# Performance work log

Measured on AMD Instinct MI355X. Metric: run time of the kernel, lower is better.

The kernel has to match this reference:

```python
import jax, jax.numpy as jnp
import numpy as np

NB = 50  # nb_steps
IN_D = 64
HID = 128
B = 256


def _cc_weights(nb):
    # Faithful port of UMNN compute_cc_weights (Clenshaw-Curtis quadrature)
    lam = np.arange(0, nb + 1).reshape(-1, 1).astype(np.float64)
    lam = np.cos((lam @ lam.T) * np.pi / nb)
    lam[:, 0] = 0.5
    lam[:, -1] = 0.5 * lam[:, -1]
    lam = lam * 2.0 / nb
    W = np.arange(0, nb + 1).reshape(-1, 1).astype(np.float64)
    W[np.arange(1, nb + 1, 2)] = 0
    W = 2.0 / (1.0 - W ** 2)
    W[0] = 1
    W[np.arange(1, nb + 1, 2)] = 0
    cc = (lam.T @ W)[:, 0].astype(np.float32)              # [nb+1]
    steps = np.cos(np.arange(0, nb + 1) * np.pi / nb).astype(np.float32)  # [nb+1]
    return jnp.asarray(cc), jnp.asarray(steps)


def setup_inputs() -> dict:
    key = jax.random.key(0)
    ks = jax.random.split(key, 16)
    d = {}
    d["x"] = jax.random.normal(ks[0], (B, 1), dtype=jnp.float32)
    d["h"] = jax.random.normal(ks[1], (B, IN_D - 1), dtype=jnp.float32)

    def lin(kw, kb, fan_in, fan_out):
        s = 1.0 / np.sqrt(fan_in)
        w = jax.random.uniform(kw, (fan_in, fan_out), jnp.float32, -s, s)
        b = jax.random.uniform(kb, (fan_out,), jnp.float32, -s, s)
        return w, b

    # Integrand MLP: in_d -> 128 -> 128 -> 1
    d["iw0"], d["ib0"] = lin(ks[2], ks[3], IN_D, HID)
    d["iw1"], d["ib1"] = lin(ks[4], ks[5], HID, HID)
    d["iw2"], d["ib2"] = lin(ks[6], ks[7], HID, 1)
    # Outer net: (in_d-1) -> 128 -> 128 -> 2
    d["nw0"], d["nb0"] = lin(ks[8], ks[9], IN_D - 1, HID)
    d["nw1"], d["nb1"] = lin(ks[10], ks[11], HID, HID)
    d["nw2"], d["nb2"] = lin(ks[12], ks[13], HID, 2)
    return d


def reference(x, h, iw0, ib0, iw1, ib1, iw2, ib2, nw0, nb0, nw1, nb1, nw2, nb2):
    cc, steps = _cc_weights(NB)  # [S1], [S1]
    S1 = NB + 1
    b = x.shape[0]

    # ----- outer quadrature: integral over t in [0, x] -----
    # t[b, i] = 0 + (x - 0) * (steps[i] + 1) / 2
    t = x[:, None, :] * (steps[None, :, None] + 1.0) / 2.0          # [B, S1, 1]

    # ----- inner UMNN: integral over s in [t, xmax], xmax = max(t) + 10 -----
    xmax = jnp.max(t) + 10.0
    s = t[:, :, None, :] + (xmax - t)[:, :, None, :] * (steps[None, None, :, None] + 1.0) / 2.0  # [B,S1,S1,1]

    hb = jnp.broadcast_to(h[:, None, None, :], (b, S1, S1, h.shape[1]))
    inp = jnp.concatenate([s, hb], axis=-1)                         # [B,S1,S1,in_d]

    # PostiveIntegrandNN: Lin-ReLU-Lin-ReLU-Lin-ELU, then + 1.0
    a = jax.nn.relu(inp @ iw0 + ib0)
    a = jax.nn.relu(a @ iw1 + ib1)
    f = jax.nn.elu(a @ iw2 + ib2) + 1.0                              # [B,S1,S1,1]

    # inner Clenshaw-Curtis reduction: z * (xT - x0) / 2
    inner = jnp.sum(f * cc[None, None, :, None], axis=2) * (xmax - t) / 2.0   # [B,S1,1]

    # outer reduction: integral from 0 to x
    outer = jnp.sum(inner * cc[None, :, None], axis=1) * x / 2.0    # [B,1]

    # outer dense net on h -> offset / scaling
    o = jax.nn.relu(h @ nw0 + nb0)
    o = jax.nn.relu(o @ nw1 + nb1)
    o = o @ nw2 + nb2                                               # [B,2]
    offset = o[:, 0:1]
    scaling = jnp.exp(o[:, 1:2])
    return scaling * outer + offset
```

## Files before the change

kernel.cpp:

```cpp
#include <hip/hip_runtime.h>
#include <math.h>

#define NBQ 50
#define S1 51
#define NPTS 2601
#define IN_D 64
#define HID 128
#define BSZ 256
#define NCHUNK 4
#define NUMAX 41

typedef __bf16 bf16x8 __attribute__((ext_vector_type(8)));
typedef float  f32x4  __attribute__((ext_vector_type(4)));

#define WS_CC     0
#define WS_STEPS  64
#define WS_XMAX   128
#define WS_BASE   256
#define WS_SCAL   33024
#define WS_OFF    33280
#define WS_PART   33536
#define WS_W1BF   41728

__global__ void k_prep(const float* __restrict__ x, const float* __restrict__ h,
                       const float* __restrict__ iw0, const float* __restrict__ ib0,
                       const float* __restrict__ iw1,
                       const float* __restrict__ nw0, const float* __restrict__ nb0,
                       const float* __restrict__ nw1, const float* __restrict__ nb1,
                       const float* __restrict__ nw2, const float* __restrict__ nb2,
                       float* __restrict__ ws) {
    int blk = blockIdx.x;
    int tid = threadIdx.x;

    if (blk < 64) {
        int idx  = blk * 256 + tid;
        int e    = idx & 7;
        int lane = (idx >> 3) & 63;
        int fk   = idx >> 9;
        int kk   = fk & 3;
        int nt   = fk >> 2;
        int k = kk * 32 + (lane >> 4) * 8 + e;
        int n = nt * 16 + (lane & 15);
        __bf16* w1bf = (__bf16*)(ws + WS_W1BF);
        w1bf[idx] = (__bf16)iw1[k * HID + n];
        return;
    }

    __shared__ float s_steps[S1];
    __shared__ float s_red[4];
    __shared__ float s_h[IN_D - 1];
    __shared__ float s_o0[HID];
    __shared__ float s_part[4];

    if (blk == 64) {
        int t = tid;
        if (t < S1) {
            double st = cos((double)t * M_PI / (double)NBQ);
            s_steps[t] = (float)st;
            ws[WS_STEPS + t] = (float)st;
            double acc = 0.0;
            for (int i = 0; i <= NBQ; ++i) {
                double Wi;
                if (i == 0)       Wi = 1.0;
                else if (i & 1)   Wi = 0.0;
                else              Wi = 2.0 / (1.0 - (double)i * (double)i);
                double lam;
                if (t == 0)  lam = 0.5;
                else         lam = cos((double)i * (double)t * M_PI / (double)NBQ);
                if (t == NBQ) lam *= 0.5;
                lam *= 2.0 / (double)NBQ;
                acc += lam * Wi;
            }
            ws[WS_CC + t] = (float)acc;
        }
        __syncthreads();
        float xb = x[t];
        float m = -1e30f;
        for (int i = 0; i < S1; ++i)
            m = fmaxf(m, xb * (s_steps[i] + 1.0f) * 0.5f);
        for (int off = 32; off > 0; off >>= 1)
            m = fmaxf(m, __shfl_down(m, off));
        if ((t & 63) == 0) s_red[t >> 6] = m;
        __syncthreads();
        if (t == 0) {
            float mm = fmaxf(fmaxf(s_red[0], s_red[1]), fmaxf(s_red[2], s_red[3]));
            ws[WS_XMAX] = mm + 10.0f;
        }
        return;
    }

    int b = blk - 65;
    int n = tid;
    bool act = (n < HID);
    if (act && n < IN_D - 1) s_h[n] = h[b * (IN_D - 1) + n];
    __syncthreads();
    float o1 = 0.0f;
    if (act) {
        float aB0 = ib0[n], aB1 = 0.f, aB2 = 0.f, aB3 = 0.f;
        float a00 = nb0[n], a01 = 0.f, a02 = 0.f, a03 = 0.f;
        int d = 0;
        for (; d + 4 <= IN_D - 1; d += 4) {
            float h0 = s_h[d], h1 = s_h[d + 1], h2 = s_h[d + 2], h3 = s_h[d + 3];
            aB0 = fmaf(h0, iw0[(1 + d) * HID + n], aB0);
            aB1 = fmaf(h1, iw0[(2 + d) * HID + n], aB1);
            aB2 = fmaf(h2, iw0[(3 + d) * HID + n], aB2);
            aB3 = fmaf(h3, iw0[(4 + d) * HID + n], aB3);
            a00 = fmaf(h0, nw0[(d)     * HID + n], a00);
            a01 = fmaf(h1, nw0[(d + 1) * HID + n], a01);
            a02 = fmaf(h2, nw0[(d + 2) * HID + n], a02);
            a03 = fmaf(h3, nw0[(d + 3) * HID + n], a03);
        }
        for (; d < IN_D - 1; ++d) {
            float hv = s_h[d];
            aB0 = fmaf(hv, iw0[(1 + d) * HID + n], aB0);
            a00 = fmaf(hv, nw0[d * HID + n], a00);
        }
        float accB = (aB0 + aB1) + (aB2 + aB3);
        float acc0 = (a00 + a01) + (a02 + a03);
        ws[WS_BASE + b * HID + n] = accB;
        s_o0[n] = fmaxf(acc0, 0.0f);
    }
    __syncthreads();
    if (act) {
        float a0 = nb1[n], a1 = 0.f, a2 = 0.f, a3 = 0.f;
        for (int m = 0; m < HID; m += 4) {
            a0 = fmaf(s_o0[m],     nw1[(m)     * HID + n], a0);
            a1 = fmaf(s_o0[m + 1], nw1[(m + 1) * HID + n], a1);
            a2 = fmaf(s_o0[m + 2], nw1[(m + 2) * HID + n], a2);
            a3 = fmaf(s_o0[m + 3], nw1[(m + 3) * HID + n], a3);
        }
        o1 = fmaxf((a0 + a1) + (a2 + a3), 0.0f);
    }
    float p0 = act ? o1 * nw2[n * 2 + 0] : 0.0f;
    float p1 = act ? o1 * nw2[n * 2 + 1] : 0.0f;
    for (int off = 32; off > 0; off >>= 1) {
        p0 += __shfl_down(p0, off);
        p1 += __shfl_down(p1, off);
    }
    int lane = tid & 63, w = tid >> 6;
    if (lane == 0 && w < 2) { s_part[w * 2] = p0; s_part[w * 2 + 1] = p1; }
    __syncthreads();
    if (tid == 0) {
        ws[WS_OFF + b]  = s_part[0] + s_part[2] + nb2[0];
        ws[WS_SCAL + b] = expf(s_part[1] + s_part[3] + nb2[1]);
    }
}

__global__ __launch_bounds__(256, 4) void k3_mfma(
        const float* __restrict__ x,
        const float* __restrict__ iw0,
        const float* __restrict__ ib1,
        const float* __restrict__ iw2,
        const float* __restrict__ ib2,
        float* __restrict__ ws) {
    __shared__ bf16x8 bfr_lds[4][4][64];
    __shared__ float zlds[4][NUMAX][17];
    __shared__ float s_tbl[NUMAX][16];
    __shared__ float w_tbl[NUMAX][16];

    int blk  = blockIdx.x;
    int b    = blk >> 2;
    int c    = blk & 3;
    int tid  = threadIdx.x;
    int wave = tid >> 6;
    int lane = tid & 63;
    int col  = lane & 15;
    int g    = lane >> 4;

    float xmax = ws[WS_XMAX];
    float xb   = x[b];
    float b2   = ib2[0];

    int NU = (c < 3) ? 41 : 40;
    int G  = (NU + 3) >> 2;

    for (int e = tid; e < NU * 16; e += 256) {
        int u  = e >> 4;
        int cl = e & 15;
        int p  = (c + 4 * u) * 16 + cl;
        int pc = (p < NPTS) ? p : (NPTS - 1);
        int i  = (int)(((unsigned)pc * 10281u) >> 19);
        int j  = pc - i * 51;
        float sti = ws[WS_STEPS + i];
        float stj = ws[WS_STEPS + j];
        float ti  = xb * (sti + 1.0f) * 0.5f;
        float w   = xmax - ti;
        s_tbl[u][cl] = fmaf(w, (stj + 1.0f) * 0.5f, ti);
        w_tbl[u][cl] = ws[WS_CC + i] * ws[WS_CC + j] * w;
    }

    const bf16x8* w1f = (const bf16x8*)(ws + WS_W1BF);
    bf16x8 Af[2][4];
#pragma unroll
    for (int nt = 0; nt < 2; ++nt) {
        int NT = wave * 2 + nt;
#pragma unroll
        for (int kk = 0; kk < 4; ++kk)
            Af[nt][kk] = w1f[(NT * 4 + kk) * 64 + lane];
    }

    const float* basep = ws + WS_BASE + b * HID;
    int m0 = wave * 32 + g * 8;
    f32x4 w0a = *(const f32x4*)(iw0 + m0);
    f32x4 w0b = *(const f32x4*)(iw0 + m0 + 4);
    f32x4 bsa = *(const f32x4*)(basep + m0);
    f32x4 bsb = *(const f32x4*)(basep + m0 + 4);

    f32x4 accInit[2], iw2v[2];
#pragma unroll
    for (int nt = 0; nt < 2; ++nt) {
        int n0 = (wave * 2 + nt) * 16 + g * 4;
        accInit[nt] = *(const f32x4*)(ib1 + n0);
        iw2v[nt]    = *(const f32x4*)(iw2 + n0);
    }

    __syncthreads();

    for (int grp = 0; grp < G; ++grp) {
        int ubase = grp * 4;
#pragma unroll
        for (int t = 0; t < 4; ++t) {
            int u = ubase + t;
            if (u < NU) {
                float s = s_tbl[u][col];
                bf16x8 bfr;
#pragma unroll
                for (int e = 0; e < 4; ++e) {
                    bfr[e]     = (__bf16)fmaxf(fmaf(s, w0a[e], bsa[e]), 0.0f);
                    bfr[4 + e] = (__bf16)fmaxf(fmaf(s, w0b[e], bsb[e]), 0.0f);
                }
                bfr_lds[t][wave][lane] = bfr;
            }
        }
        __syncthreads();
#pragma unroll
        for (int t = 0; t < 4; ++t) {
            int u = ubase + t;
            if (u < NU) {
                bf16x8 f0 = bfr_lds[t][0][lane];
                bf16x8 f1 = bfr_lds[t][1][lane];
                bf16x8 f2 = bfr_lds[t][2][lane];
                bf16x8 f3 = bfr_lds[t][3][lane];
                __builtin_amdgcn_s_setprio(1);
                f32x4 a0 = __builtin_amdgcn_mfma_f32_16x16x32_bf16(Af[0][0], f0, accInit[0], 0, 0, 0);
                f32x4 a1 = __builtin_amdgcn_mfma_f32_16x16x32_bf16(Af[1][0], f0, accInit[1], 0, 0, 0);
                a0 = __builtin_amdgcn_mfma_f32_16x16x32_bf16(Af[0][1], f1, a0, 0, 0, 0);
                a1 = __builtin_amdgcn_mfma_f32_16x16x32_bf16(Af[1][1], f1, a1, 0, 0, 0);
                a0 = __builtin_amdgcn_mfma_f32_16x16x32_bf16(Af[0][2], f2, a0, 0, 0, 0);
                a1 = __builtin_amdgcn_mfma_f32_16x16x32_bf16(Af[1][2], f2, a1, 0, 0, 0);
                a0 = __builtin_amdgcn_mfma_f32_16x16x32_bf16(Af[0][3], f3, a0, 0, 0, 0);
                a1 = __builtin_amdgcn_mfma_f32_16x16x32_bf16(Af[1][3], f3, a1, 0, 0, 0);
                __builtin_amdgcn_s_setprio(0);

                float za = 0.f, zb = 0.f;
#pragma unroll
                for (int q = 0; q < 4; ++q) {
                    za = fmaf(fmaxf(a0[q], 0.0f), iw2v[0][q], za);
                    zb = fmaf(fmaxf(a1[q], 0.0f), iw2v[1][q], zb);
                }
                float z = za + zb;
                z += __shfl_xor(z, 16);
                z += __shfl_xor(z, 32);
                if (lane < 16) zlds[wave][u][lane] = z;
            }
        }
        __syncthreads();
    }

    float vsum = 0.0f;
    int npass = (NU + 15) >> 4;
    for (int pass = 0; pass < npass; ++pass) {
        int u = pass * 16 + wave * 4 + g;
        if (u < NU) {
            int p = (c + 4 * u) * 16 + col;
            if (p < NPTS) {
                float z = zlds[0][u][col] + zlds[1][u][col]
                        + zlds[2][u][col] + zlds[3][u][col] + b2;
                float f = (z > 0.0f) ? (z + 1.0f) : __expf(z);
                vsum += w_tbl[u][col] * f;
            }
        }
    }
#pragma unroll
    for (int off = 1; off < 64; off <<= 1)
        vsum += __shfl_xor(vsum, off);
    if (lane == 0)
        ws[WS_PART + blk * 4 + wave] = vsum * 0.5f;
}

__global__ void k4_final(const float* __restrict__ x, const float* __restrict__ ws,
                         float* __restrict__ out) {
    int b = threadIdx.x;
    float sum = 0.0f;
#pragma unroll
    for (int c = 0; c < 16; ++c) sum += ws[WS_PART + b * 16 + c];
    out[b] = ws[WS_SCAL + b] * sum * x[b] * 0.5f + ws[WS_OFF + b];
}

extern "C" void kernel_launch(void* const* d_in, const int* in_sizes, int n_in,
                              void* d_out, int out_size, void* d_ws, size_t ws_size,
                              hipStream_t stream) {
    const float* x   = (const float*)d_in[0];
    const float* h   = (const float*)d_in[1];
    const float* iw0 = (const float*)d_in[2];
    const float* ib0 = (const float*)d_in[3];
    const float* iw1 = (const float*)d_in[4];
    const float* ib1 = (const float*)d_in[5];
    const float* iw2 = (const float*)d_in[6];
    const float* ib2 = (const float*)d_in[7];
    const float* nw0 = (const float*)d_in[8];
    const float* nb0 = (const float*)d_in[9];
    const float* nw1 = (const float*)d_in[10];
    const float* nb1 = (const float*)d_in[11];
    const float* nw2 = (const float*)d_in[12];
    const float* nb2 = (const float*)d_in[13];
    float* ws  = (float*)d_ws;
    float* out = (float*)d_out;

    hipLaunchKernelGGL(k_prep, dim3(64 + 1 + BSZ), dim3(256), 0, stream,
                       x, h, iw0, ib0, iw1, nw0, nb0, nw1, nb1, nw2, nb2, ws);
    hipLaunchKernelGGL(k3_mfma, dim3(BSZ * NCHUNK), dim3(256), 0, stream,
                       x, iw0, ib1, iw2, ib2, ws);
    hipLaunchKernelGGL(k4_final, dim3(1), dim3(BSZ), 0, stream, x, ws, out);
}
```

Baseline: 49.44 us.

## Give each wave a whole quadrature tile and double-buffer the layer-1 fragments

Re-partitions the second-layer MFMA work so each wave computes all 8 output n-tiles for one 16-point group, instead of every wave computing 2 n-tiles for all 4 groups. This keeps the whole bf16 W1 in registers and removes the cross-wave z reduction through LDS along with the separate final pass. Layer-1 activations for the next group are built into a second LDS buffer while the current group is processed, leaving one barrier per group. The final output weights are pre-converted to bf16 in the prep kernel. In exchange, register pressure rises and the launch bound drops to 2 blocks per SM, which reduces occupancy.

```diff
diff --git a/kernel.cpp b/kernel.cpp
--- a/kernel.cpp
+++ b/kernel.cpp
@@ -12,19 +12,28 @@
 
 typedef __bf16 bf16x8 __attribute__((ext_vector_type(8)));
 typedef float  f32x4  __attribute__((ext_vector_type(4)));
+typedef unsigned int u32x2 __attribute__((ext_vector_type(2)));
 
 #define WS_CC     0
 #define WS_STEPS  64
 #define WS_XMAX   128
+#define WS_IW2BF  192
 #define WS_BASE   256
 #define WS_SCAL   33024
 #define WS_OFF    33280
 #define WS_PART   33536
 #define WS_W1BF   41728
 
+static __device__ inline float hi_f32(unsigned int u) {
+    return __builtin_bit_cast(float, u & 0xffff0000u);
+}
+static __device__ inline float lo_f32(unsigned int u) {
+    return __builtin_bit_cast(float, u << 16);
+}
+
 __global__ void k_prep(const float* __restrict__ x, const float* __restrict__ h,
                        const float* __restrict__ iw0, const float* __restrict__ ib0,
-                       const float* __restrict__ iw1,
+                       const float* __restrict__ iw1, const float* __restrict__ iw2,
                        const float* __restrict__ nw0, const float* __restrict__ nb0,
                        const float* __restrict__ nw1, const float* __restrict__ nb1,
                        const float* __restrict__ nw2, const float* __restrict__ nb2,
@@ -54,6 +63,10 @@
 
     if (blk == 64) {
         int t = tid;
+        if (t < HID) {
+            __bf16* iw2bf = (__bf16*)(ws + WS_IW2BF);
+            iw2bf[t] = (__bf16)iw2[t];
+        }
         if (t < S1) {
             double st = cos((double)t * M_PI / (double)NBQ);
             s_steps[t] = (float)st;
@@ -115,10 +128,8 @@
             aB0 = fmaf(hv, iw0[(1 + d) * HID + n], aB0);
             a00 = fmaf(hv, nw0[d * HID + n], a00);
         }
-        float accB = (aB0 + aB1) + (aB2 + aB3);
-        float acc0 = (a00 + a01) + (a02 + a03);
-        ws[WS_BASE + b * HID + n] = accB;
-        s_o0[n] = fmaxf(acc0, 0.0f);
+        ws[WS_BASE + b * HID + n] = (aB0 + aB1) + (aB2 + aB3);
+        s_o0[n] = fmaxf((a00 + a01) + (a02 + a03), 0.0f);
     }
     __syncthreads();
     if (act) {
@@ -146,17 +157,16 @@
     }
 }
 
-__global__ __launch_bounds__(256, 4) void k3_mfma(
+__global__ __launch_bounds__(256, 2) void k3_mfma(
         const float* __restrict__ x,
         const float* __restrict__ iw0,
         const float* __restrict__ ib1,
-        const float* __restrict__ iw2,
         const float* __restrict__ ib2,
         float* __restrict__ ws) {
-    __shared__ bf16x8 bfr_lds[4][4][64];
-    __shared__ float zlds[4][NUMAX][17];
+    __shared__ bf16x8 bfr[2][4][4][64];
     __shared__ float s_tbl[NUMAX][16];
     __shared__ float w_tbl[NUMAX][16];
+    __shared__ float s_red[4];
 
     int blk  = blockIdx.x;
     int b    = blk >> 2;
@@ -186,17 +196,24 @@
         float ti  = xb * (sti + 1.0f) * 0.5f;
         float w   = xmax - ti;
         s_tbl[u][cl] = fmaf(w, (stj + 1.0f) * 0.5f, ti);
-        w_tbl[u][cl] = ws[WS_CC + i] * ws[WS_CC + j] * w;
+        w_tbl[u][cl] = (p < NPTS) ? ws[WS_CC + i] * ws[WS_CC + j] * w : 0.0f;
     }
 
     const bf16x8* w1f = (const bf16x8*)(ws + WS_W1BF);
-    bf16x8 Af[2][4];
-#pragma unroll
-    for (int nt = 0; nt < 2; ++nt) {
-        int NT = wave * 2 + nt;
+    bf16x8 Af[8][4];
+#pragma unroll
+    for (int nt = 0; nt < 8; ++nt)
 #pragma unroll
         for (int kk = 0; kk < 4; ++kk)
-            Af[nt][kk] = w1f[(NT * 4 + kk) * 64 + lane];
+            Af[nt][kk] = w1f[(nt * 4 + kk) * 64 + lane];
+
+    f32x4 ib1v[8];
+    u32x2 iwp[8];
+    const unsigned int* iw2p = (const unsigned int*)(ws + WS_IW2BF);
+#pragma unroll
+    for (int nt = 0; nt < 8; ++nt) {
+        ib1v[nt] = *(const f32x4*)(ib1 + nt * 16 + g * 4);
+        iwp[nt]  = *(const u32x2*)(iw2p + nt * 8 + g * 2);
     }
 
     const float* basep = ws + WS_BASE + b * HID;
@@ -206,86 +223,91 @@
     f32x4 bsa = *(const f32x4*)(basep + m0);
     f32x4 bsb = *(const f32x4*)(basep + m0 + 4);
 
-    f32x4 accInit[2], iw2v[2];
-#pragma unroll
-    for (int nt = 0; nt < 2; ++nt) {
-        int n0 = (wave * 2 + nt) * 16 + g * 4;
-        accInit[nt] = *(const f32x4*)(ib1 + n0);
-        iw2v[nt]    = *(const f32x4*)(iw2 + n0);
-    }
-
-    __syncthreads();
+    __syncthreads();
+
+#pragma unroll
+    for (int t = 0; t < 4; ++t) {
+        int u = t;
+        if (u < NU) {
+            float s = s_tbl[u][col];
+            bf16x8 fr;
+#pragma unroll
+            for (int e = 0; e < 4; ++e) {
+                fr[e]     = (__bf16)fmaxf(fmaf(s, w0a[e], bsa[e]), 0.0f);
+                fr[4 + e] = (__bf16)fmaxf(fmaf(s, w0b[e], bsb[e]), 0.0f);
+            }
+            bfr[0][t][wave][lane] = fr;
+        }
+    }
+    __syncthreads();
+
+    float vsum = 0.0f;
 
     for (int grp = 0; grp < G; ++grp) {
-        int ubase = grp * 4;
-#pragma unroll
-        for (int t = 0; t < 4; ++t) {
-            int u = ubase + t;
-            if (u < NU) {
-                float s = s_tbl[u][col];
-                bf16x8 bfr;
-#pragma unroll
-                for (int e = 0; e < 4; ++e) {
-                    bfr[e]     = (__bf16)fmaxf(fmaf(s, w0a[e], bsa[e]), 0.0f);
-                    bfr[4 + e] = (__bf16)fmaxf(fmaf(s, w0b[e], bsb[e]), 0.0f);
+        int buf = grp & 1;
+        if (grp + 1 < G) {
+#pragma unroll
+            for (int t = 0; t < 4; ++t) {
+                int u = (grp + 1) * 4 + t;
+                if (u < NU) {
+                    float s = s_tbl[u][col];
+                    bf16x8 fr;
+#pragma unroll
+                    for (int e = 0; e < 4; ++e) {
+                        fr[e]     = (__bf16)fmaxf(fmaf(s, w0a[e], bsa[e]), 0.0f);
+                        fr[4 + e] = (__bf16)fmaxf(fmaf(s, w0b[e], bsb[e]), 0.0f);
+                    }
+                    bfr[buf ^ 1][t][wave][lane] = fr;
                 }
-                bfr_lds[t][wave][lane] = bfr;
             }
         }
+        int u = grp * 4 + wave;
+        if (u < NU) {
+            bf16x8 f0 = bfr[buf][wave][0][lane];
+            bf16x8 f1 = bfr[buf][wave][1][lane];
+            f32x4 acc[8];
+            __builtin_amdgcn_s_setprio(1);
+#pragma unroll
+            for (int nt = 0; nt < 8; ++nt)
+                acc[nt] = __builtin_amdgcn_mfma_f32_16x16x32_bf16(Af[nt][0], f0, ib1v[nt], 0, 0, 0);
+            bf16x8 f2 = bfr[buf][wave][2][lane];
+#pragma unroll
+            for (int nt = 0; nt < 8; ++nt)
+                acc[nt] = __builtin_amdgcn_mfma_f32_16x16x32_bf16(Af[nt][1], f1, acc[nt], 0, 0, 0);
+            bf16x8 f3 = bfr[buf][wave][3][lane];
+#pragma unroll
+            for (int nt = 0; nt < 8; ++nt)
+                acc[nt] = __builtin_amdgcn_mfma_f32_16x16x32_bf16(Af[nt][2], f2, acc[nt], 0, 0, 0);
+#pragma unroll
+            for (int nt = 0; nt < 8; ++nt)
+                acc[nt] = __builtin_amdgcn_mfma_f32_16x16x32_bf16(Af[nt][3], f3, acc[nt], 0, 0, 0);
+            __builtin_amdgcn_s_setprio(0);
+
+            float z0 = 0.f, z1 = 0.f, z2 = 0.f, z3 = 0.f;
+#pragma unroll
+            for (int nt = 0; nt < 8; ++nt) {
+                z0 = fmaf(fmaxf(acc[nt][0], 0.0f), lo_f32(iwp[nt][0]), z0);
+                z1 = fmaf(fmaxf(acc[nt][1], 0.0f), hi_f32(iwp[nt][0]), z1);
+                z2 = fmaf(fmaxf(acc[nt][2], 0.0f), lo_f32(iwp[nt][1]), z2);
+                z3 = fmaf(fmaxf(acc[nt][3], 0.0f), hi_f32(iwp[nt][1]), z3);
+            }
+            float z = (z0 + z1) + (z2 + z3);
+            z += __shfl_xor(z, 16);
+            z += __shfl_xor(z, 32);
+            z += b2;
+            float f = (z > 0.0f) ? (z + 1.0f) : __expf(z);
+            vsum += w_tbl[u][col] * f;
+        }
         __syncthreads();
-#pragma unroll
-        for (int t = 0; t < 4; ++t) {
-            int u = ubase + t;
-            if (u < NU) {
-                bf16x8 f0 = bfr_lds[t][0][lane];
-                bf16x8 f1 = bfr_lds[t][1][lane];
-                bf16x8 f2 = bfr_lds[t][2][lane];
-                bf16x8 f3 = bfr_lds[t][3][lane];
-                __builtin_amdgcn_s_setprio(1);
-                f32x4 a0 = __builtin_amdgcn_mfma_f32_16x16x32_bf16(Af[0][0], f0, accInit[0], 0, 0, 0);
-                f32x4 a1 = __builtin_amdgcn_mfma_f32_16x16x32_bf16(Af[1][0], f0, accInit[1], 0, 0, 0);
-                a0 = __builtin_amdgcn_mfma_f32_16x16x32_bf16(Af[0][1], f1, a0, 0, 0, 0);
-                a1 = __builtin_amdgcn_mfma_f32_16x16x32_bf16(Af[1][1], f1, a1, 0, 0, 0);
-                a0 = __builtin_amdgcn_mfma_f32_16x16x32_bf16(Af[0][2], f2, a0, 0, 0, 0);
-                a1 = __builtin_amdgcn_mfma_f32_16x16x32_bf16(Af[1][2], f2, a1, 0, 0, 0);
-                a0 = __builtin_amdgcn_mfma_f32_16x16x32_bf16(Af[0][3], f3, a0, 0, 0, 0);
-                a1 = __builtin_amdgcn_mfma_f32_16x16x32_bf16(Af[1][3], f3, a1, 0, 0, 0);
-                __builtin_amdgcn_s_setprio(0);
-
-                float za = 0.f, zb = 0.f;
-#pragma unroll
-                for (int q = 0; q < 4; ++q) {
-                    za = fmaf(fmaxf(a0[q], 0.0f), iw2v[0][q], za);
-                    zb = fmaf(fmaxf(a1[q], 0.0f), iw2v[1][q], zb);
-                }
-                float z = za + zb;
-                z += __shfl_xor(z, 16);
-                z += __shfl_xor(z, 32);
-                if (lane < 16) zlds[wave][u][lane] = z;
-            }
-        }
-        __syncthreads();
-    }
-
-    float vsum = 0.0f;
-    int npass = (NU + 15) >> 4;
-    for (int pass = 0; pass < npass; ++pass) {
-        int u = pass * 16 + wave * 4 + g;
-        if (u < NU) {
-            int p = (c + 4 * u) * 16 + col;
-            if (p < NPTS) {
-                float z = zlds[0][u][col] + zlds[1][u][col]
-                        + zlds[2][u][col] + zlds[3][u][col] + b2;
-                float f = (z > 0.0f) ? (z + 1.0f) : __expf(z);
-                vsum += w_tbl[u][col] * f;
-            }
-        }
-    }
+    }
+
 #pragma unroll
     for (int off = 1; off < 64; off <<= 1)
         vsum += __shfl_xor(vsum, off);
-    if (lane == 0)
-        ws[WS_PART + blk * 4 + wave] = vsum * 0.5f;
+    if (lane == 0) s_red[wave] = vsum;
+    __syncthreads();
+    if (tid == 0)
+        ws[WS_PART + blk] = (s_red[0] + s_red[1] + s_red[2] + s_red[3]) * 0.125f;
 }
 
 __global__ void k4_final(const float* __restrict__ x, const float* __restrict__ ws,
@@ -293,7 +315,7 @@
     int b = threadIdx.x;
     float sum = 0.0f;
 #pragma unroll
-    for (int c = 0; c < 16; ++c) sum += ws[WS_PART + b * 16 + c];
+    for (int c = 0; c < NCHUNK; ++c) sum += ws[WS_PART + b * NCHUNK + c];
     out[b] = ws[WS_SCAL + b] * sum * x[b] * 0.5f + ws[WS_OFF + b];
 }
 
@@ -318,8 +340,8 @@
     float* out = (float*)d_out;
 
     hipLaunchKernelGGL(k_prep, dim3(64 + 1 + BSZ), dim3(256), 0, stream,
-                       x, h, iw0, ib0, iw1, nw0, nb0, nw1, nb1, nw2, nb2, ws);
+                       x, h, iw0, ib0, iw1, iw2, nw0, nb0, nw1, nb1, nw2, nb2, ws);
     hipLaunchKernelGGL(k3_mfma, dim3(BSZ * NCHUNK), dim3(256), 0, stream,
-                       x, iw0, ib1, iw2, ib2, ws);
+                       x, iw0, ib1, ib2, ws);
     hipLaunchKernelGGL(k4_final, dim3(1), dim3(BSZ), 0, stream, x, ws, out);
 }
```

New measurement: 57.24 us. 1.16x slower.
